# Optimization experiments

Measured on AMD Instinct MI355X. Metric: run time of the kernel, lower is better.

## Reference

```python
import jax, jax.numpy as jnp
import numpy as np

BN_EPS = 1e-5

def setup_inputs() -> dict:
    key = jax.random.key(0)
    ks = jax.random.split(key, 6)
    B, C, H, W, Hd = 16, 512, 64, 64, 128
    return {
        "x": jax.random.normal(ks[0], (B, C, H, W), dtype=jnp.float32),
        "wA": jax.random.normal(ks[1], (Hd, C), dtype=jnp.float32) * 0.05,
        "wB": jax.random.normal(ks[2], (Hd, C), dtype=jnp.float32) * 0.05,
        "wC": jax.random.normal(ks[3], (Hd, C), dtype=jnp.float32) * 0.05,
        "wProj": jax.random.normal(ks[4], (C, Hd), dtype=jnp.float32) * 0.05,
        "bn_gamma": jnp.ones((C,), dtype=jnp.float32),
        "bn_beta": jnp.zeros((C,), dtype=jnp.float32),
        "bn_mean": jnp.zeros((C,), dtype=jnp.float32),
        "bn_var": jnp.ones((C,), dtype=jnp.float32),
    }

def reference(x, wA, wB, wC, wProj, bn_gamma, bn_beta, bn_mean, bn_var):
    B, C, H, W = x.shape
    N = H * W
    xf = x.reshape(B, C, N)                                  # [B, C, N]
    # three 1x1 convs (bias-free) == channel-mixing matmuls
    A = jax.nn.softmax(jnp.einsum('hc,bcn->bhn', wA, xf), axis=2)   # [B, Hd, N]
    Bf = jnp.einsum('hc,bcn->bhn', wB, xf)                          # [B, Hd, N]
    Cs = jax.nn.softmax(jnp.einsum('hc,bcn->bhn', wC, xf), axis=2)  # [B, Hd, N]
    # FeatureGathering = B_feat @ A^T : [B, Hd, Hd]
    G = jnp.einsum('bhn,bgn->bhg', Bf, A)
    # distribute: G @ C_softmax -> [B, Hd, N]
    y = jnp.einsum('bhg,bgn->bhn', G, Cs)
    # projection back to C channels + inference-mode BatchNorm
    p = jnp.einsum('ch,bhn->bcn', wProj, y)                         # [B, C, N]
    inv = jax.lax.rsqrt(bn_var + BN_EPS)
    out = (p - bn_mean[None, :, None]) * (inv * bn_gamma)[None, :, None] + bn_beta[None, :, None]
    return out.reshape(B, C, H, W)
```

## Files before the change

kernel.cpp:

```cpp
#include <hip/hip_runtime.h>
#include <cstddef>

#define NPIX 4096
#define CDIM 512

typedef _Float16 half8 __attribute__((ext_vector_type(8)));
typedef float f32x4 __attribute__((ext_vector_type(4)));

__device__ __forceinline__ void gl_lds16(const void* g, void* l) {
    __builtin_amdgcn_global_load_lds(
        (const __attribute__((address_space(1))) void*)g,
        (__attribute__((address_space(3))) void*)l, 16, 0, 0);
}

__global__ __launch_bounds__(256)
void prep_w(const float* __restrict__ wA, const float* __restrict__ wB,
            const float* __restrict__ wC, _Float16* __restrict__ Wh)
{
    const int gid  = blockIdx.x * 256 + threadIdx.x;
    const int lane = gid & 63;
    const int frag = gid >> 6;
    const int msub = frag & 7, kt = (frag >> 3) & 15, mt = frag >> 7;
    const float* __restrict__ W = (mt == 0) ? wA : (mt == 1) ? wB : wC;
    const int m  = msub * 16 + (lane & 15);
    const int c0 = kt * 32 + ((lane >> 4) << 3);
    const float* src = W + m * CDIM + c0;
    union { _Float16 h[8]; float4 f; } u;
#pragma unroll
    for (int j = 0; j < 8; ++j) u.h[j] = (_Float16)src[j];
    *(float4*)(Wh + (size_t)frag * 512 + lane * 8) = u.f;
}

__global__ __launch_bounds__(256)
void m_to_h(const float* __restrict__ M, _Float16* __restrict__ Mh)
{
    const int gid  = blockIdx.x * 256 + threadIdx.x;
    const int lane = gid & 63;
    const int frag = gid >> 6;
    const int msub = frag & 7, kt = (frag >> 3) & 3, ct = (frag >> 5) & 3, b = frag >> 7;
    const float* src = M + ((size_t)b * 512 + ct * 128 + msub * 16 + (lane & 15)) * 128
                         + kt * 32 + ((lane >> 4) << 3);
    union { _Float16 h[8]; float4 f; } u;
#pragma unroll
    for (int j = 0; j < 8; ++j) u.h[j] = (_Float16)src[j];
    *(float4*)(Mh + (size_t)frag * 512 + lane * 8) = u.f;
}

__global__ __launch_bounds__(256)
void conv_mfma(const float* __restrict__ x, const _Float16* __restrict__ Wh,
               float* __restrict__ P)
{
    const int nt = blockIdx.x, mt = blockIdx.y, b = blockIdx.z;
    const int tid  = threadIdx.x;
    const int wave = tid >> 6, lane = tid & 63;
    const int wm = wave >> 1, wn = wave & 1;

    __shared__ alignas(16) _Float16 sA[4096];
    __shared__ alignas(16) _Float16 sB[128 * 40];

    f32x4 acc[4][4];
#pragma unroll
    for (int i = 0; i < 4; ++i)
#pragma unroll
        for (int j = 0; j < 4; ++j)
#pragma unroll
            for (int e = 0; e < 4; ++e) acc[i][j][e] = 0.f;

    const int n0 = (tid & 31) << 2;
    const int k0 = (tid >> 5) << 2;
    const float* xb = x + ((size_t)b << 21) + (nt << 7) + n0;
    const _Float16* WhB = Wh + (size_t)mt * 128 * 512;

    for (int kt = 0; kt < 16; ++kt) {
#pragma unroll
        for (int s = 0; s < 2; ++s) {
            const int frag = wave + (s << 2);
            gl_lds16(WhB + ((size_t)kt * 8 + frag) * 512 + lane * 8, &sA[frag * 512]);
        }
        const float* xs = xb + (size_t)(kt * 32 + k0) * NPIX;
        float ld[4][4];
        *(float4*)&ld[0][0] = *(const float4*)(xs);
        *(float4*)&ld[1][0] = *(const float4*)(xs + NPIX);
        *(float4*)&ld[2][0] = *(const float4*)(xs + 2 * NPIX);
        *(float4*)&ld[3][0] = *(const float4*)(xs + 3 * NPIX);
#pragma unroll
        for (int c = 0; c < 4; ++c) {
            const int n    = n0 + c;
            const int blkh = ((k0 >> 2) ^ (((n >> 4) & 3) << 1)) << 2;
            union { _Float16 h[4]; float2 f; } u;
            u.h[0] = (_Float16)ld[0][c];
            u.h[1] = (_Float16)ld[1][c];
            u.h[2] = (_Float16)ld[2][c];
            u.h[3] = (_Float16)ld[3][c];
            *(float2*)&sB[n * 40 + blkh] = u.f;
        }
        __syncthreads();

        half8 av[4], bv[4];
#pragma unroll
        for (int i = 0; i < 4; ++i)
            av[i] = *(const half8*)&sA[(((wm << 2) + i) << 9) + (lane << 3)];
#pragma unroll
        for (int j = 0; j < 4; ++j) {
            const int nj = (wn << 6) + (j << 4) + (lane & 15);
            const int qs = ((lane >> 4) ^ ((nj >> 4) & 3)) << 3;
            bv[j] = *(const half8*)&sB[nj * 40 + qs];
        }
#pragma unroll
        for (int i = 0; i < 4; ++i)
#pragma unroll
            for (int j = 0; j < 4; ++j)
                acc[i][j] = __builtin_amdgcn_mfma_f32_16x16x32_f16(av[i], bv[j], acc[i][j], 0, 0, 0);
        __syncthreads();
    }

    float* Pb = P + (((size_t)b * 384 + mt * 128) << 12) + (nt << 7);
#pragma unroll
    for (int i = 0; i < 4; ++i) {
        const int row0 = (wm << 6) + (i << 4) + ((lane >> 4) << 2);
#pragma unroll
        for (int j = 0; j < 4; ++j) {
            const int col = (wn << 6) + (j << 4) + (lane & 15);
#pragma unroll
            for (int r = 0; r < 4; ++r)
                Pb[(size_t)(row0 + r) * NPIX + col] = acc[i][j][r];
        }
    }
}

__global__ __launch_bounds__(256)
void softmax_rows(float* __restrict__ P)
{
    const int blk = blockIdx.x;
    const int b   = blk >> 8;
    const int r   = blk & 255;
    const int m   = (r < 128) ? r : (r + 128);
    float* row = P + ((size_t)b * 384 + m) * NPIX;
    const int tid = threadIdx.x;

    float4 v[4];
    float mx = -3.402823466e38f;
#pragma unroll
    for (int j = 0; j < 4; ++j) {
        v[j] = *(const float4*)(row + j * 1024 + tid * 4);
        mx = fmaxf(mx, fmaxf(fmaxf(v[j].x, v[j].y), fmaxf(v[j].z, v[j].w)));
    }
#pragma unroll
    for (int o = 32; o > 0; o >>= 1) mx = fmaxf(mx, __shfl_xor(mx, o));
    __shared__ float redm[4];
    __shared__ float reds[4];
    const int wid = tid >> 6, lane = tid & 63;
    if (lane == 0) redm[wid] = mx;
    __syncthreads();
    mx = fmaxf(fmaxf(redm[0], redm[1]), fmaxf(redm[2], redm[3]));

    float s = 0.f;
#pragma unroll
    for (int j = 0; j < 4; ++j) {
        v[j].x = __expf(v[j].x - mx);
        v[j].y = __expf(v[j].y - mx);
        v[j].z = __expf(v[j].z - mx);
        v[j].w = __expf(v[j].w - mx);
        s += (v[j].x + v[j].y) + (v[j].z + v[j].w);
    }
#pragma unroll
    for (int o = 32; o > 0; o >>= 1) s += __shfl_xor(s, o);
    if (lane == 0) reds[wid] = s;
    __syncthreads();
    s = (reds[0] + reds[1]) + (reds[2] + reds[3]);
    const float inv = 1.f / s;
#pragma unroll
    for (int j = 0; j < 4; ++j) {
        v[j].x *= inv; v[j].y *= inv; v[j].z *= inv; v[j].w *= inv;
        *(float4*)(row + j * 1024 + tid * 4) = v[j];
    }
}

__global__ __launch_bounds__(256)
void g_partial(const float* __restrict__ P, float* __restrict__ Gp)
{
    const int kc = blockIdx.x;
    const int b  = blockIdx.y;
    const float* __restrict__ Arow = P + (size_t)b * 384 * NPIX;
    const float* __restrict__ Brow = Arow + (size_t)128 * NPIX;

    __shared__ float Hs[16][132];
    __shared__ float Gs[16][132];

    const int tid = threadIdx.x;
    const int tr  = tid >> 4;
    const int tc  = tid & 15;

    float acc[8][8];
#pragma unroll
    for (int i = 0; i < 8; ++i)
#pragma unroll
        for (int j = 0; j < 8; ++j) acc[i][j] = 0.f;

    for (int kt = 0; kt < 256; kt += 16) {
        const int nb = kc * 256 + kt;
#pragma unroll
        for (int l = 0; l < 2; ++l) {
            int idx = tid + l * 256;
            int rr  = idx >> 2;
            int k4  = (idx & 3) << 2;
            float4 v = *(const float4*)(Brow + (size_t)rr * NPIX + nb + k4);
            Hs[k4 + 0][rr] = v.x; Hs[k4 + 1][rr] = v.y;
            Hs[k4 + 2][rr] = v.z; Hs[k4 + 3][rr] = v.w;
            float4 u = *(const float4*)(Arow + (size_t)rr * NPIX + nb + k4);
            Gs[k4 + 0][rr] = u.x; Gs[k4 + 1][rr] = u.y;
            Gs[k4 + 2][rr] = u.z; Gs[k4 + 3][rr] = u.w;
        }
        __syncthreads();
#pragma unroll
        for (int kk = 0; kk < 16; ++kk) {
            float h8[8], g8[8];
            *(float4*)(&h8[0]) = *(const float4*)(&Hs[kk][tr * 8]);
            *(float4*)(&h8[4]) = *(const float4*)(&Hs[kk][tr * 8 + 4]);
            *(float4*)(&g8[0]) = *(const float4*)(&Gs[kk][tc * 8]);
            *(float4*)(&g8[4]) = *(const float4*)(&Gs[kk][tc * 8 + 4]);
#pragma unroll
            for (int i = 0; i < 8; ++i)
#pragma unroll
                for (int j = 0; j < 8; ++j) acc[i][j] = fmaf(h8[i], g8[j], acc[i][j]);
        }
        __syncthreads();
    }

    float* O = Gp + ((size_t)b * 16 + kc) * 16384;
#pragma unroll
    for (int i = 0; i < 8; ++i) {
        float* row = O + (size_t)(tr * 8 + i) * 128 + tc * 8;
        *(float4*)(row)     = *(float4*)(&acc[i][0]);
        *(float4*)(row + 4) = *(float4*)(&acc[i][4]);
    }
}

__global__ __launch_bounds__(256)
void g_reduce(const float* __restrict__ Gp, float* __restrict__ G)
{
    const int t    = blockIdx.x * 256 + threadIdx.x;
    const int flat = t * 4;
    const int b    = flat >> 14;
    const int rr   = flat & 16383;
    const float* base = Gp + (size_t)b * 16 * 16384 + rr;
    float4 s = make_float4(0.f, 0.f, 0.f, 0.f);
#pragma unroll
    for (int kc = 0; kc < 16; ++kc) {
        float4 v = *(const float4*)(base + (size_t)kc * 16384);
        s.x += v.x; s.y += v.y; s.z += v.z; s.w += v.w;
    }
    *(float4*)(G + (size_t)b * 16384 + rr) = s;
}

__global__ __launch_bounds__(256)
void proj_g(const float* __restrict__ G, const float* __restrict__ wProj,
            float* __restrict__ M)
{
    const int ct = blockIdx.x;
    const int b  = blockIdx.y;
    __shared__ float Gs[16384];
    const int tid = threadIdx.x;
    const float* Gb = G + (size_t)b * 16384;
#pragma unroll
    for (int l = 0; l < 16; ++l) {
        int i4 = (tid + l * 256) * 4;
        *(float4*)(&Gs[i4]) = *(const float4*)(Gb + i4);
    }
    __syncthreads();
    const int g  = tid & 127;
    const int cl = tid >> 7;
    const int c0 = ct * 32 + cl;
    float acc[16];
#pragma unroll
    for (int i = 0; i < 16; ++i) acc[i] = 0.f;
    for (int h = 0; h < 128; ++h) {
        const float gv = Gs[h * 128 + g];
#pragma unroll
        for (int cc = 0; cc < 16; ++cc)
            acc[cc] = fmaf(wProj[(size_t)(c0 + cc * 2) * 128 + h], gv, acc[cc]);
    }
    float* Mb = M + (size_t)b * 512 * 128;
#pragma unroll
    for (int cc = 0; cc < 16; ++cc)
        Mb[(size_t)(c0 + cc * 2) * 128 + g] = acc[cc];
}

__global__ __launch_bounds__(256)
void final_mfma(const float* __restrict__ P, const _Float16* __restrict__ Mh,
                const float* __restrict__ gamma, const float* __restrict__ beta,
                const float* __restrict__ mean,  const float* __restrict__ var,
                float* __restrict__ out)
{
    const int nt = blockIdx.x, ct = blockIdx.y, b = blockIdx.z;
    const int tid  = threadIdx.x;
    const int wave = tid >> 6, lane = tid & 63;
    const int wm = wave >> 1, wn = wave & 1;

    __shared__ alignas(16) _Float16 sA[4096];
    __shared__ alignas(16) _Float16 sB[128 * 40];

    f32x4 acc[4][4];
#pragma unroll
    for (int i = 0; i < 4; ++i)
#pragma unroll
        for (int j = 0; j < 4; ++j)
#pragma unroll
            for (int e = 0; e < 4; ++e) acc[i][j][e] = 0.f;

    const int n0 = (tid & 31) << 2;
    const int k0 = (tid >> 5) << 2;
    const float* Cs = P + (((size_t)b * 384 + 256) << 12) + (nt << 7) + n0;
    const _Float16* MhB = Mh + (size_t)(b * 4 + ct) * 4 * 8 * 512;

    for (int kt = 0; kt < 4; ++kt) {
#pragma unroll
        for (int s = 0; s < 2; ++s) {
            const int frag = wave + (s << 2);
            gl_lds16(MhB + ((size_t)kt * 8 + frag) * 512 + lane * 8, &sA[frag * 512]);
        }
        const float* cs = Cs + (size_t)(kt * 32 + k0) * NPIX;
        float ld[4][4];
        *(float4*)&ld[0][0] = *(const float4*)(cs);
        *(float4*)&ld[1][0] = *(const float4*)(cs + NPIX);
        *(float4*)&ld[2][0] = *(const float4*)(cs + 2 * NPIX);
        *(float4*)&ld[3][0] = *(const float4*)(cs + 3 * NPIX);
#pragma unroll
        for (int c = 0; c < 4; ++c) {
            const int n    = n0 + c;
            const int blkh = ((k0 >> 2) ^ (((n >> 4) & 3) << 1)) << 2;
            union { _Float16 h[4]; float2 f; } u;
            u.h[0] = (_Float16)ld[0][c];
            u.h[1] = (_Float16)ld[1][c];
            u.h[2] = (_Float16)ld[2][c];
            u.h[3] = (_Float16)ld[3][c];
            *(float2*)&sB[n * 40 + blkh] = u.f;
        }
        __syncthreads();

        half8 av[4], bv[4];
#pragma unroll
        for (int i = 0; i < 4; ++i)
            av[i] = *(const half8*)&sA[(((wm << 2) + i) << 9) + (lane << 3)];
#pragma unroll
        for (int j = 0; j < 4; ++j) {
            const int nj = (wn << 6) + (j << 4) + (lane & 15);
            const int qs = ((lane >> 4) ^ ((nj >> 4) & 3)) << 3;
            bv[j] = *(const half8*)&sB[nj * 40 + qs];
        }
#pragma unroll
        for (int i = 0; i < 4; ++i)
#pragma unroll
            for (int j = 0; j < 4; ++j)
                acc[i][j] = __builtin_amdgcn_mfma_f32_16x16x32_f16(av[i], bv[j], acc[i][j], 0, 0, 0);
        __syncthreads();
    }

    float* ob = out + (((size_t)b << 9) << 12);
#pragma unroll
    for (int i = 0; i < 4; ++i) {
        const int rc = (ct << 7) + (wm << 6) + (i << 4) + ((lane >> 4) << 2);
#pragma unroll
        for (int r = 0; r < 4; ++r) {
            const int c   = rc + r;
            const float s = gamma[c] * rsqrtf(var[c] + 1e-5f);
            const float t = fmaf(-mean[c], s, beta[c]);
            float* row = ob + ((size_t)c << 12) + (nt << 7);
#pragma unroll
            for (int j = 0; j < 4; ++j) {
                const int col = (wn << 6) + (j << 4) + (lane & 15);
                row[col] = fmaf(acc[i][j][r], s, t);
            }
        }
    }
}

extern "C" void kernel_launch(void* const* d_in, const int* in_sizes, int n_in,
                              void* d_out, int out_size, void* d_ws, size_t ws_size,
                              hipStream_t stream)
{
    const float* x     = (const float*)d_in[0];
    const float* wA    = (const float*)d_in[1];
    const float* wB    = (const float*)d_in[2];
    const float* wC    = (const float*)d_in[3];
    const float* wProj = (const float*)d_in[4];
    const float* gamma = (const float*)d_in[5];
    const float* beta  = (const float*)d_in[6];
    const float* mean  = (const float*)d_in[7];
    const float* var   = (const float*)d_in[8];
    float* out = (float*)d_out;

    char* ws = (char*)d_ws;
    float*     P  = (float*)(ws);
    float*     Gp = (float*)(ws + 100663296);
    float*     G  = (float*)(ws + 117440512);
    float*     M  = (float*)(ws + 118489088);
    _Float16*  Wh = (_Float16*)(ws + 122683392);
    _Float16*  Mh = (_Float16*)(ws + 123076608);

    prep_w     <<<dim3(96),        256, 0, stream>>>(wA, wB, wC, Wh);
    conv_mfma  <<<dim3(32, 3, 16), 256, 0, stream>>>(x, Wh, P);
    softmax_rows<<<dim3(4096),     256, 0, stream>>>(P);
    g_partial  <<<dim3(16, 16),    256, 0, stream>>>(P, Gp);
    g_reduce   <<<dim3(256),       256, 0, stream>>>(Gp, G);
    proj_g     <<<dim3(16, 16),    256, 0, stream>>>(G, wProj, M);
    m_to_h     <<<dim3(512),       256, 0, stream>>>(M, Mh);
    final_mfma <<<dim3(32, 4, 16), 256, 0, stream>>>(P, Mh, gamma, beta, mean, var, out);
}
```

Before: 386.1 us.

## Store intermediates in fp16 and move G and projection GEMMs to MFMA

```diff
diff --git a/kernel.cpp b/kernel.cpp
--- a/kernel.cpp
+++ b/kernel.cpp
@@ -4,8 +4,9 @@
 #define NPIX 4096
 #define CDIM 512
 
-typedef _Float16 half8 __attribute__((ext_vector_type(8)));
-typedef float f32x4 __attribute__((ext_vector_type(4)));
+typedef _Float16 half8  __attribute__((ext_vector_type(8)));
+typedef _Float16 half4v __attribute__((ext_vector_type(4)));
+typedef float    f32x4  __attribute__((ext_vector_type(4)));
 
 __device__ __forceinline__ void gl_lds16(const void* g, void* l) {
     __builtin_amdgcn_global_load_lds(
@@ -32,23 +33,21 @@
 }
 
 __global__ __launch_bounds__(256)
-void m_to_h(const float* __restrict__ M, _Float16* __restrict__ Mh)
-{
-    const int gid  = blockIdx.x * 256 + threadIdx.x;
-    const int lane = gid & 63;
-    const int frag = gid >> 6;
-    const int msub = frag & 7, kt = (frag >> 3) & 3, ct = (frag >> 5) & 3, b = frag >> 7;
-    const float* src = M + ((size_t)b * 512 + ct * 128 + msub * 16 + (lane & 15)) * 128
-                         + kt * 32 + ((lane >> 4) << 3);
+void prep_wp(const float* __restrict__ wProj, _Float16* __restrict__ WpH)
+{
+    const int gid = blockIdx.x * 256 + threadIdx.x;
+    const int i8  = gid * 8;
+    float4 a = *(const float4*)(wProj + i8);
+    float4 b = *(const float4*)(wProj + i8 + 4);
     union { _Float16 h[8]; float4 f; } u;
-#pragma unroll
-    for (int j = 0; j < 8; ++j) u.h[j] = (_Float16)src[j];
-    *(float4*)(Mh + (size_t)frag * 512 + lane * 8) = u.f;
+    u.h[0]=(_Float16)a.x; u.h[1]=(_Float16)a.y; u.h[2]=(_Float16)a.z; u.h[3]=(_Float16)a.w;
+    u.h[4]=(_Float16)b.x; u.h[5]=(_Float16)b.y; u.h[6]=(_Float16)b.z; u.h[7]=(_Float16)b.w;
+    *(float4*)(WpH + i8) = u.f;
 }
 
 __global__ __launch_bounds__(256)
 void conv_mfma(const float* __restrict__ x, const _Float16* __restrict__ Wh,
-               float* __restrict__ P)
+               _Float16* __restrict__ P)
 {
     const int nt = blockIdx.x, mt = blockIdx.y, b = blockIdx.z;
     const int tid  = threadIdx.x;
@@ -114,7 +113,7 @@
         __syncthreads();
     }
 
-    float* Pb = P + (((size_t)b * 384 + mt * 128) << 12) + (nt << 7);
+    _Float16* Pb = P + (((size_t)b * 384 + mt * 128) << 12) + (nt << 7);
 #pragma unroll
     for (int i = 0; i < 4; ++i) {
         const int row0 = (wm << 6) + (i << 4) + ((lane >> 4) << 2);
@@ -123,28 +122,28 @@
             const int col = (wn << 6) + (j << 4) + (lane & 15);
 #pragma unroll
             for (int r = 0; r < 4; ++r)
-                Pb[(size_t)(row0 + r) * NPIX + col] = acc[i][j][r];
-        }
-    }
-}
-
-__global__ __launch_bounds__(256)
-void softmax_rows(float* __restrict__ P)
+                Pb[(size_t)(row0 + r) * NPIX + col] = (_Float16)acc[i][j][r];
+        }
+    }
+}
+
+__global__ __launch_bounds__(256)
+void softmax_rows(_Float16* __restrict__ P)
 {
     const int blk = blockIdx.x;
     const int b   = blk >> 8;
     const int r   = blk & 255;
     const int m   = (r < 128) ? r : (r + 128);
-    float* row = P + ((size_t)b * 384 + m) * NPIX;
+    _Float16* row = P + (((size_t)b * 384 + m) << 12);
     const int tid = threadIdx.x;
 
-    float4 v[4];
+    half8 h[2];
+    float v[16];
+    h[0] = *(const half8*)(row + tid * 16);
+    h[1] = *(const half8*)(row + tid * 16 + 8);
     float mx = -3.402823466e38f;
 #pragma unroll
-    for (int j = 0; j < 4; ++j) {
-        v[j] = *(const float4*)(row + j * 1024 + tid * 4);
-        mx = fmaxf(mx, fmaxf(fmaxf(v[j].x, v[j].y), fmaxf(v[j].z, v[j].w)));
-    }
+    for (int j = 0; j < 16; ++j) { v[j] = (float)h[j >> 3][j & 7]; mx = fmaxf(mx, v[j]); }
 #pragma unroll
     for (int o = 32; o > 0; o >>= 1) mx = fmaxf(mx, __shfl_xor(mx, o));
     __shared__ float redm[4];
@@ -156,13 +155,7 @@
 
     float s = 0.f;
 #pragma unroll
-    for (int j = 0; j < 4; ++j) {
-        v[j].x = __expf(v[j].x - mx);
-        v[j].y = __expf(v[j].y - mx);
-        v[j].z = __expf(v[j].z - mx);
-        v[j].w = __expf(v[j].w - mx);
-        s += (v[j].x + v[j].y) + (v[j].z + v[j].w);
-    }
+    for (int j = 0; j < 16; ++j) { v[j] = __expf(v[j] - mx); s += v[j]; }
 #pragma unroll
     for (int o = 32; o > 0; o >>= 1) s += __shfl_xor(s, o);
     if (lane == 0) reds[wid] = s;
@@ -170,124 +163,140 @@
     s = (reds[0] + reds[1]) + (reds[2] + reds[3]);
     const float inv = 1.f / s;
 #pragma unroll
-    for (int j = 0; j < 4; ++j) {
-        v[j].x *= inv; v[j].y *= inv; v[j].z *= inv; v[j].w *= inv;
-        *(float4*)(row + j * 1024 + tid * 4) = v[j];
-    }
-}
-
-__global__ __launch_bounds__(256)
-void g_partial(const float* __restrict__ P, float* __restrict__ Gp)
-{
-    const int kc = blockIdx.x;
-    const int b  = blockIdx.y;
-    const float* __restrict__ Arow = P + (size_t)b * 384 * NPIX;
-    const float* __restrict__ Brow = Arow + (size_t)128 * NPIX;
-
-    __shared__ float Hs[16][132];
-    __shared__ float Gs[16][132];
-
-    const int tid = threadIdx.x;
-    const int tr  = tid >> 4;
-    const int tc  = tid & 15;
-
-    float acc[8][8];
-#pragma unroll
-    for (int i = 0; i < 8; ++i)
-#pragma unroll
-        for (int j = 0; j < 8; ++j) acc[i][j] = 0.f;
-
-    for (int kt = 0; kt < 256; kt += 16) {
-        const int nb = kc * 256 + kt;
-#pragma unroll
-        for (int l = 0; l < 2; ++l) {
-            int idx = tid + l * 256;
-            int rr  = idx >> 2;
-            int k4  = (idx & 3) << 2;
-            float4 v = *(const float4*)(Brow + (size_t)rr * NPIX + nb + k4);
-            Hs[k4 + 0][rr] = v.x; Hs[k4 + 1][rr] = v.y;
-            Hs[k4 + 2][rr] = v.z; Hs[k4 + 3][rr] = v.w;
-            float4 u = *(const float4*)(Arow + (size_t)rr * NPIX + nb + k4);
-            Gs[k4 + 0][rr] = u.x; Gs[k4 + 1][rr] = u.y;
-            Gs[k4 + 2][rr] = u.z; Gs[k4 + 3][rr] = u.w;
-        }
-        __syncthreads();
-#pragma unroll
-        for (int kk = 0; kk < 16; ++kk) {
-            float h8[8], g8[8];
-            *(float4*)(&h8[0]) = *(const float4*)(&Hs[kk][tr * 8]);
-            *(float4*)(&h8[4]) = *(const float4*)(&Hs[kk][tr * 8 + 4]);
-            *(float4*)(&g8[0]) = *(const float4*)(&Gs[kk][tc * 8]);
-            *(float4*)(&g8[4]) = *(const float4*)(&Gs[kk][tc * 8 + 4]);
-#pragma unroll
-            for (int i = 0; i < 8; ++i)
-#pragma unroll
-                for (int j = 0; j < 8; ++j) acc[i][j] = fmaf(h8[i], g8[j], acc[i][j]);
-        }
-        __syncthreads();
-    }
-
-    float* O = Gp + ((size_t)b * 16 + kc) * 16384;
-#pragma unroll
-    for (int i = 0; i < 8; ++i) {
-        float* row = O + (size_t)(tr * 8 + i) * 128 + tc * 8;
-        *(float4*)(row)     = *(float4*)(&acc[i][0]);
-        *(float4*)(row + 4) = *(float4*)(&acc[i][4]);
-    }
-}
-
-__global__ __launch_bounds__(256)
-void g_reduce(const float* __restrict__ Gp, float* __restrict__ G)
-{
-    const int t    = blockIdx.x * 256 + threadIdx.x;
-    const int flat = t * 4;
-    const int b    = flat >> 14;
-    const int rr   = flat & 16383;
-    const float* base = Gp + (size_t)b * 16 * 16384 + rr;
-    float4 s = make_float4(0.f, 0.f, 0.f, 0.f);
+    for (int j = 0; j < 16; ++j) h[j >> 3][j & 7] = (_Float16)(v[j] * inv);
+    *(half8*)(row + tid * 16)     = h[0];
+    *(half8*)(row + tid * 16 + 8) = h[1];
+}
+
+__global__ __launch_bounds__(256)
+void g_partial_mfma(const _Float16* __restrict__ P, float* __restrict__ Gp)
+{
+    const int kc = blockIdx.x, b = blockIdx.y;
+    const int tid  = threadIdx.x;
+    const int wave = tid >> 6, lane = tid & 63;
+    const int wm = wave >> 1, wn = wave & 1;
+
+    const _Float16* Pa = P + ((size_t)b * 384 << 12);
+    const _Float16* Pf = Pa + ((size_t)128 << 12);
+
+    f32x4 acc[4][4];
+#pragma unroll
+    for (int i = 0; i < 4; ++i)
+#pragma unroll
+        for (int j = 0; j < 4; ++j)
+#pragma unroll
+            for (int e = 0; e < 4; ++e) acc[i][j][e] = 0.f;
+
+    const int klane = ((lane >> 4) << 3);
+    const int rlane = lane & 15;
+#pragma unroll 2
+    for (int kt = 0; kt < 8; ++kt) {
+        const int k = (kc << 8) + (kt << 5) + klane;
+        half8 av[4], bv[4];
+#pragma unroll
+        for (int i = 0; i < 4; ++i)
+            av[i] = *(const half8*)(Pa + ((size_t)((wm << 6) + (i << 4) + rlane) << 12) + k);
+#pragma unroll
+        for (int j = 0; j < 4; ++j)
+            bv[j] = *(const half8*)(Pf + ((size_t)((wn << 6) + (j << 4) + rlane) << 12) + k);
+#pragma unroll
+        for (int i = 0; i < 4; ++i)
+#pragma unroll
+            for (int j = 0; j < 4; ++j)
+                acc[i][j] = __builtin_amdgcn_mfma_f32_16x16x32_f16(av[i], bv[j], acc[i][j], 0, 0, 0);
+    }
+
+    float* O = Gp + (((size_t)b * 16 + kc) << 14);
+#pragma unroll
+    for (int i = 0; i < 4; ++i) {
+        const int row0 = (wm << 6) + (i << 4) + ((lane >> 4) << 2);
+#pragma unroll
+        for (int j = 0; j < 4; ++j) {
+            const int col = (wn << 6) + (j << 4) + rlane;
+#pragma unroll
+            for (int r = 0; r < 4; ++r)
+                O[(size_t)(row0 + r) * 128 + col] = acc[i][j][r];
+        }
+    }
+}
+
+__global__ __launch_bounds__(256)
+void g_reduce_cvt(const float* __restrict__ Gp, _Float16* __restrict__ Gt)
+{
+    const int gid  = blockIdx.x * 256 + threadIdx.x;
+    const int i8   = gid * 8;
+    const int b    = i8 >> 14;
+    const int rr   = i8 & 16383;
+    const float* base = Gp + ((size_t)b << 18) + rr;
+    float s[8];
+#pragma unroll
+    for (int e = 0; e < 8; ++e) s[e] = 0.f;
 #pragma unroll
     for (int kc = 0; kc < 16; ++kc) {
-        float4 v = *(const float4*)(base + (size_t)kc * 16384);
-        s.x += v.x; s.y += v.y; s.z += v.z; s.w += v.w;
-    }
-    *(float4*)(G + (size_t)b * 16384 + rr) = s;
-}
-
-__global__ __launch_bounds__(256)
-void proj_g(const float* __restrict__ G, const float* __restrict__ wProj,
-            float* __restrict__ M)
-{
-    const int ct = blockIdx.x;
-    const int b  = blockIdx.y;
-    __shared__ float Gs[16384];
-    const int tid = threadIdx.x;
-    const float* Gb = G + (size_t)b * 16384;
-#pragma unroll
-    for (int l = 0; l < 16; ++l) {
-        int i4 = (tid + l * 256) * 4;
-        *(float4*)(&Gs[i4]) = *(const float4*)(Gb + i4);
-    }
-    __syncthreads();
-    const int g  = tid & 127;
-    const int cl = tid >> 7;
-    const int c0 = ct * 32 + cl;
-    float acc[16];
-#pragma unroll
-    for (int i = 0; i < 16; ++i) acc[i] = 0.f;
-    for (int h = 0; h < 128; ++h) {
-        const float gv = Gs[h * 128 + g];
-#pragma unroll
-        for (int cc = 0; cc < 16; ++cc)
-            acc[cc] = fmaf(wProj[(size_t)(c0 + cc * 2) * 128 + h], gv, acc[cc]);
-    }
-    float* Mb = M + (size_t)b * 512 * 128;
-#pragma unroll
-    for (int cc = 0; cc < 16; ++cc)
-        Mb[(size_t)(c0 + cc * 2) * 128 + g] = acc[cc];
-}
-
-__global__ __launch_bounds__(256)
-void final_mfma(const float* __restrict__ P, const _Float16* __restrict__ Mh,
+        float4 v0 = *(const float4*)(base + ((size_t)kc << 14));
+        float4 v1 = *(const float4*)(base + ((size_t)kc << 14) + 4);
+        s[0]+=v0.x; s[1]+=v0.y; s[2]+=v0.z; s[3]+=v0.w;
+        s[4]+=v1.x; s[5]+=v1.y; s[6]+=v1.z; s[7]+=v1.w;
+    }
+    union { _Float16 h[8]; float4 f; } u;
+#pragma unroll
+    for (int e = 0; e < 8; ++e) u.h[e] = (_Float16)s[e];
+    *(float4*)(Gt + ((size_t)b << 14) + rr) = u.f;
+}
+
+__global__ __launch_bounds__(256)
+void proj_mfma(const _Float16* __restrict__ WpH, const _Float16* __restrict__ Gt,
+               _Float16* __restrict__ Mh)
+{
+    const int ct = blockIdx.x, b = blockIdx.y;
+    const int tid  = threadIdx.x;
+    const int wave = tid >> 6, lane = tid & 63;
+    const int wm = wave >> 1, wn = wave & 1;
+
+    f32x4 acc[4][4];
+#pragma unroll
+    for (int i = 0; i < 4; ++i)
+#pragma unroll
+        for (int j = 0; j < 4; ++j)
+#pragma unroll
+            for (int e = 0; e < 4; ++e) acc[i][j][e] = 0.f;
+
+    const int klane = ((lane >> 4) << 3);
+    const int rlane = lane & 15;
+    const _Float16* Gb = Gt + ((size_t)b << 14);
+#pragma unroll
+    for (int kt = 0; kt < 4; ++kt) {
+        const int k = (kt << 5) + klane;
+        half8 av[4], bv[4];
+#pragma unroll
+        for (int i = 0; i < 4; ++i)
+            av[i] = *(const half8*)(WpH + (size_t)((ct << 7) + (wm << 6) + (i << 4) + rlane) * 128 + k);
+#pragma unroll
+        for (int j = 0; j < 4; ++j)
+            bv[j] = *(const half8*)(Gb + (size_t)((wn << 6) + (j << 4) + rlane) * 128 + k);
+#pragma unroll
+        for (int i = 0; i < 4; ++i)
+#pragma unroll
+            for (int j = 0; j < 4; ++j)
+                acc[i][j] = __builtin_amdgcn_mfma_f32_16x16x32_f16(av[i], bv[j], acc[i][j], 0, 0, 0);
+    }
+
+    _Float16* Mb = Mh + ((size_t)b << 16);
+#pragma unroll
+    for (int i = 0; i < 4; ++i) {
+        const int row0 = (ct << 7) + (wm << 6) + (i << 4) + ((lane >> 4) << 2);
+#pragma unroll
+        for (int j = 0; j < 4; ++j) {
+            const int col = (wn << 6) + (j << 4) + rlane;
+#pragma unroll
+            for (int r = 0; r < 4; ++r)
+                Mb[(size_t)(row0 + r) * 128 + col] = (_Float16)acc[i][j][r];
+        }
+    }
+}
+
+__global__ __launch_bounds__(256)
+void final_mfma(const _Float16* __restrict__ P, const _Float16* __restrict__ Mh,
                 const float* __restrict__ gamma, const float* __restrict__ beta,
                 const float* __restrict__ mean,  const float* __restrict__ var,
                 float* __restrict__ out)
@@ -297,7 +306,6 @@
     const int wave = tid >> 6, lane = tid & 63;
     const int wm = wave >> 1, wn = wave & 1;
 
-    __shared__ alignas(16) _Float16 sA[4096];
     __shared__ alignas(16) _Float16 sB[128 * 40];
 
     f32x4 acc[4][4];
@@ -310,41 +318,33 @@
 
     const int n0 = (tid & 31) << 2;
     const int k0 = (tid >> 5) << 2;
-    const float* Cs = P + (((size_t)b * 384 + 256) << 12) + (nt << 7) + n0;
-    const _Float16* MhB = Mh + (size_t)(b * 4 + ct) * 4 * 8 * 512;
+    const int klane = ((lane >> 4) << 3);
+    const int rlane = lane & 15;
+    const _Float16* Cs  = P + (((size_t)b * 384 + 256) << 12) + (nt << 7) + n0;
+    const _Float16* MhB = Mh + ((size_t)b << 16) + ((size_t)(ct << 7) << 7);
 
     for (int kt = 0; kt < 4; ++kt) {
-#pragma unroll
-        for (int s = 0; s < 2; ++s) {
-            const int frag = wave + (s << 2);
-            gl_lds16(MhB + ((size_t)kt * 8 + frag) * 512 + lane * 8, &sA[frag * 512]);
-        }
-        const float* cs = Cs + (size_t)(kt * 32 + k0) * NPIX;
-        float ld[4][4];
-        *(float4*)&ld[0][0] = *(const float4*)(cs);
-        *(float4*)&ld[1][0] = *(const float4*)(cs + NPIX);
-        *(float4*)&ld[2][0] = *(const float4*)(cs + 2 * NPIX);
-        *(float4*)&ld[3][0] = *(const float4*)(cs + 3 * NPIX);
+        const _Float16* cs = Cs + ((size_t)((kt << 5) + k0) << 12);
+        half4v ld0 = *(const half4v*)(cs);
+        half4v ld1 = *(const half4v*)(cs + NPIX);
+        half4v ld2 = *(const half4v*)(cs + 2 * NPIX);
+        half4v ld3 = *(const half4v*)(cs + 3 * NPIX);
 #pragma unroll
         for (int c = 0; c < 4; ++c) {
             const int n    = n0 + c;
             const int blkh = ((k0 >> 2) ^ (((n >> 4) & 3) << 1)) << 2;
-            union { _Float16 h[4]; float2 f; } u;
-            u.h[0] = (_Float16)ld[0][c];
-            u.h[1] = (_Float16)ld[1][c];
-            u.h[2] = (_Float16)ld[2][c];
-            u.h[3] = (_Float16)ld[3][c];
-            *(float2*)&sB[n * 40 + blkh] = u.f;
+            half4v col = { ld0[c], ld1[c], ld2[c], ld3[c] };
+            *(half4v*)&sB[n * 40 + blkh] = col;
         }
         __syncthreads();
 
         half8 av[4], bv[4];
 #pragma unroll
         for (int i = 0; i < 4; ++i)
-            av[i] = *(const half8*)&sA[(((wm << 2) + i) << 9) + (lane << 3)];
+            av[i] = *(const half8*)(MhB + (size_t)((wm << 6) + (i << 4) + rlane) * 128 + (kt << 5) + klane);
 #pragma unroll
         for (int j = 0; j < 4; ++j) {
-            const int nj = (wn << 6) + (j << 4) + (lane & 15);
+            const int nj = (wn << 6) + (j << 4) + rlane;
             const int qs = ((lane >> 4) ^ ((nj >> 4) & 3)) << 3;
             bv[j] = *(const half8*)&sB[nj * 40 + qs];
         }
@@ -368,7 +368,7 @@
             float* row = ob + ((size_t)c << 12) + (nt << 7);
 #pragma unroll
             for (int j = 0; j < 4; ++j) {
-                const int col = (wn << 6) + (j << 4) + (lane & 15);
+                const int col = (wn << 6) + (j << 4) + rlane;
                 row[col] = fmaf(acc[i][j][r], s, t);
             }
         }
@@ -391,19 +391,19 @@
     float* out = (float*)d_out;
 
     char* ws = (char*)d_ws;
-    float*     P  = (float*)(ws);
-    float*     Gp = (float*)(ws + 100663296);
-    float*     G  = (float*)(ws + 117440512);
-    float*     M  = (float*)(ws + 118489088);
-    _Float16*  Wh = (_Float16*)(ws + 122683392);
-    _Float16*  Mh = (_Float16*)(ws + 123076608);
-
-    prep_w     <<<dim3(96),        256, 0, stream>>>(wA, wB, wC, Wh);
-    conv_mfma  <<<dim3(32, 3, 16), 256, 0, stream>>>(x, Wh, P);
-    softmax_rows<<<dim3(4096),     256, 0, stream>>>(P);
-    g_partial  <<<dim3(16, 16),    256, 0, stream>>>(P, Gp);
-    g_reduce   <<<dim3(256),       256, 0, stream>>>(Gp, G);
-    proj_g     <<<dim3(16, 16),    256, 0, stream>>>(G, wProj, M);
-    m_to_h     <<<dim3(512),       256, 0, stream>>>(M, Mh);
-    final_mfma <<<dim3(32, 4, 16), 256, 0, stream>>>(P, Mh, gamma, beta, mean, var, out);
-}
+    _Float16* P   = (_Float16*)(ws);
+    float*    Gp  = (float*)(ws + 50331648);
+    _Float16* Gt  = (_Float16*)(ws + 67108864);
+    _Float16* WpH = (_Float16*)(ws + 67633152);
+    _Float16* Mh  = (_Float16*)(ws + 67764224);
+    _Float16* Wh  = (_Float16*)(ws + 69861376);
+
+    prep_w        <<<dim3(96),        256, 0, stream>>>(wA, wB, wC, Wh);
+    prep_wp       <<<dim3(32),        256, 0, stream>>>(wProj, WpH);
+    conv_mfma     <<<dim3(32, 3, 16), 256, 0, stream>>>(x, Wh, P);
+    softmax_rows  <<<dim3(4096),      256, 0, stream>>>(P);
+    g_partial_mfma<<<dim3(16, 16),    256, 0, stream>>>(P, Gp);
+    g_reduce_cvt  <<<dim3(128),       256, 0, stream>>>(Gp, Gt);
+    proj_mfma     <<<dim3(4, 16),     256, 0, stream>>>(WpH, Gt, Mh);
+    final_mfma    <<<dim3(32, 4, 16), 256, 0, stream>>>(P, Mh, gamma, beta, mean, var, out);
+}
```

Result: faster. 324.2 us (-16.0%).
